# Optimization experiments

Measured on AMD Instinct MI355X. Metric: run time of the kernel, lower is better.

The kernel has to match this reference:

```python
import jax, jax.numpy as jnp
import numpy as np

B, S, D, H = 4, 2048, 1024, 16
DK = D // H

def setup_inputs() -> dict:
    key = jax.random.key(0)
    ks = jax.random.split(key, 5)
    scale = 0.02
    return {
        "x": jax.random.normal(ks[0], (B, S, D), dtype=jnp.float32),
        "Wqkv": jax.random.normal(ks[1], (3 * D, D), dtype=jnp.float32) * scale,
        "bqkv": jax.random.normal(ks[2], (3 * D,), dtype=jnp.float32) * scale,
        "Wout": jax.random.normal(ks[3], (D, D), dtype=jnp.float32) * scale,
        "bout": jax.random.normal(ks[4], (D,), dtype=jnp.float32) * scale,
    }

def reference(x, Wqkv, bqkv, Wout, bout):
    # fused QKV projection: [B,S,3D]
    qkv = jnp.einsum('bsd,ed->bse', x, Wqkv) + bqkv
    q, k, v = jnp.split(qkv, 3, axis=-1)
    # [B,S,D] -> [B,H,S,DK]
    def heads(t):
        return t.reshape(B, S, H, DK).transpose(0, 2, 1, 3)
    q, k, v = heads(q), heads(k), heads(v)
    # scaled dot-product attention (no mask, no dropout)
    scores = jnp.einsum('bhqd,bhkd->bhqk', q, k) / jnp.sqrt(jnp.float32(DK))
    attn = jax.nn.softmax(scores, axis=-1)
    out = jnp.einsum('bhqk,bhkd->bhqd', attn, v)
    # merge heads -> [B,S,D]
    out = out.transpose(0, 2, 1, 3).reshape(B, S, D)
    return jnp.einsum('bsd,ed->bse', out, Wout) + bout
```

## Files before the change

kernel.cpp:

```cpp
#include <hip/hip_runtime.h>
#include <hip/hip_bf16.h>
#include <cstdint>
#include <cstddef>

typedef __bf16 bf16_t;
typedef bf16_t bf16x8 __attribute__((ext_vector_type(8)));
typedef bf16_t bf16x4 __attribute__((ext_vector_type(4)));
typedef bf16_t bf16x2 __attribute__((ext_vector_type(2)));
typedef float f32x4 __attribute__((ext_vector_type(4)));
typedef float f32x16 __attribute__((ext_vector_type(16)));
typedef unsigned int u32x4 __attribute__((ext_vector_type(4)));

#define B_  4
#define S_  2048
#define D_  1024
#define H_  16
#define DK_ 64

#define QSCALE 0.18033688011112042f

__device__ __forceinline__ void gload_lds16(const bf16_t* g, bf16_t* l) {
  __builtin_amdgcn_global_load_lds(
      (__attribute__((address_space(1))) void*)(void*)g,
      (__attribute__((address_space(3))) void*)(void*)l,
      16, 0, 0);
}

__device__ __forceinline__ f32x4 mfma_bf16(bf16x8 a, bf16x8 b, f32x4 c) {
  return __builtin_amdgcn_mfma_f32_16x16x32_bf16(a, b, c, 0, 0, 0);
}
__device__ __forceinline__ f32x16 mfma32(bf16x8 a, bf16x8 b, f32x16 c) {
  return __builtin_amdgcn_mfma_f32_32x32x16_bf16(a, b, c, 0, 0, 0);
}

__device__ __forceinline__ unsigned pk2(float a, float b) {
  bf16x2 v; v[0] = (bf16_t)a; v[1] = (bf16_t)b;
  return __builtin_bit_cast(unsigned, v);
}

__device__ __forceinline__ void pl32(unsigned &a, unsigned &b) {
  auto r = __builtin_amdgcn_permlane32_swap((int)a, (int)b, false, false);
  a = (unsigned)r[0];
  b = (unsigned)r[1];
}

__global__ void cvt_f32_bf16(const float* __restrict__ in, bf16_t* __restrict__ out, int n4) {
  int i = blockIdx.x * blockDim.x + threadIdx.x;
  if (i < n4) {
    float4 v = reinterpret_cast<const float4*>(in)[i];
    bf16x4 o;
    o[0] = (bf16_t)v.x; o[1] = (bf16_t)v.y; o[2] = (bf16_t)v.z; o[3] = (bf16_t)v.w;
    reinterpret_cast<bf16x4*>(out)[i] = o;
  }
}


__global__ __launch_bounds__(256) void gemm_qkv(
    const bf16_t* __restrict__ A, const bf16_t* __restrict__ Bm,
    const float* __restrict__ bias,
    bf16_t* __restrict__ Qf, bf16_t* __restrict__ Kf, bf16_t* __restrict__ Vf) {
  __shared__ bf16_t As[128 * 32];
  __shared__ bf16_t Bs[128 * 32];
  const int t = threadIdx.x;
  const int l = t & 63;
  const int w = t >> 6;
  const int wm = w >> 1, wn = w & 1;
  const int fr = l & 15, fh = l >> 4;
  const int bid = (int)blockIdx.x;
  const int swz = (bid & 7) * 192 + (bid >> 3);
  const int m0 = (swz / 24) * 128, n0 = (swz % 24) * 128;
  const int K = 1024;
  const int ar = t >> 2, ak = (t & 3) * 8;

  f32x4 acc[4][4] = {};

  for (int k0 = 0; k0 < K; k0 += 32) {
    gload_lds16(A + (size_t)(m0 + ar) * K + k0 + ak,        &As[t * 8]);
    gload_lds16(A + (size_t)(m0 + 64 + ar) * K + k0 + ak,   &As[2048 + t * 8]);
    gload_lds16(Bm + (size_t)(n0 + ar) * K + k0 + ak,       &Bs[t * 8]);
    gload_lds16(Bm + (size_t)(n0 + 64 + ar) * K + k0 + ak,  &Bs[2048 + t * 8]);
    __syncthreads();
    bf16x8 af[4], bfv[4];
#pragma unroll
    for (int i = 0; i < 4; ++i)
      af[i] = *reinterpret_cast<const bf16x8*>(&As[(wm * 64 + i * 16 + fr) * 32 + fh * 8]);
#pragma unroll
    for (int i = 0; i < 4; ++i)
      bfv[i] = *reinterpret_cast<const bf16x8*>(&Bs[(wn * 64 + i * 16 + fr) * 32 + fh * 8]);
#pragma unroll
    for (int mi = 0; mi < 4; ++mi)
#pragma unroll
      for (int ni = 0; ni < 4; ++ni)
        acc[mi][ni] = mfma_bf16(af[mi], bfv[ni], acc[mi][ni]);
    __syncthreads();
  }

#pragma unroll
  for (int mi = 0; mi < 4; ++mi) {
#pragma unroll
    for (int ni = 0; ni < 4; ++ni) {
      const int e = n0 + wn * 64 + ni * 16 + fr;
      const int sec = e >> 10;
      const int h = (e & 1023) >> 6, dk = e & 63;
      const float bv = bias[e];
#pragma unroll
      for (int j = 0; j < 4; ++j) {
        const int m = m0 + wm * 64 + mi * 16 + fh * 4 + j;
        const int b = m >> 11, s = m & 2047;
        const float val = acc[mi][ni][j] + bv;
        const size_t hb = (size_t)(b * H_ + h) * (S_ * DK_);
        if (sec == 2) {
          const int tv = s >> 5, tt = (s >> 4) & 1, jj = dk >> 5;
          const int lane = (dk & 31) + ((s >> 3) & 1) * 32, el = s & 7;
          Vf[hb + (size_t)((((tv * 2 + tt) * 2 + jj) * 64 + lane) * 8 + el)] = (bf16_t)val;
        } else {
          const int tq = s >> 5, d = dk >> 4;
          const int lane = (s & 31) + ((dk >> 3) & 1) * 32, el = dk & 7;
          const size_t idx = hb + (size_t)(((tq * 4 + d) * 64 + lane) * 8 + el);
          if (sec == 0) Qf[idx] = (bf16_t)(val * QSCALE);
          else          Kf[idx] = (bf16_t)val;
        }
      }
    }
  }
}

__global__ __launch_bounds__(256) void gemm_out(
    const bf16_t* __restrict__ A, const bf16_t* __restrict__ Bm,
    const float* __restrict__ bias, float* __restrict__ out) {
  __shared__ bf16_t As[128 * 32];
  __shared__ bf16_t Bs[128 * 32];
  const int t = threadIdx.x;
  const int l = t & 63;
  const int w = t >> 6;
  const int wm = w >> 1, wn = w & 1;
  const int fr = l & 15, fh = l >> 4;
  const int bid = (int)blockIdx.x;
  const int swz = (bid & 7) * 64 + (bid >> 3);
  const int m0 = (swz >> 3) * 128, n0 = (swz & 7) * 128;
  const int K = 1024;
  const int ar = t >> 2, ak = (t & 3) * 8;

  f32x4 acc[4][4] = {};

  for (int k0 = 0; k0 < K; k0 += 32) {
    gload_lds16(A + (size_t)(m0 + ar) * K + k0 + ak,        &As[t * 8]);
    gload_lds16(A + (size_t)(m0 + 64 + ar) * K + k0 + ak,   &As[2048 + t * 8]);
    gload_lds16(Bm + (size_t)(n0 + ar) * K + k0 + ak,       &Bs[t * 8]);
    gload_lds16(Bm + (size_t)(n0 + 64 + ar) * K + k0 + ak,  &Bs[2048 + t * 8]);
    __syncthreads();
    bf16x8 af[4], bfv[4];
#pragma unroll
    for (int i = 0; i < 4; ++i)
      af[i] = *reinterpret_cast<const bf16x8*>(&As[(wm * 64 + i * 16 + fr) * 32 + fh * 8]);
#pragma unroll
    for (int i = 0; i < 4; ++i)
      bfv[i] = *reinterpret_cast<const bf16x8*>(&Bs[(wn * 64 + i * 16 + fr) * 32 + fh * 8]);
#pragma unroll
    for (int mi = 0; mi < 4; ++mi)
#pragma unroll
      for (int ni = 0; ni < 4; ++ni)
        acc[mi][ni] = mfma_bf16(af[mi], bfv[ni], acc[mi][ni]);
    __syncthreads();
  }

#pragma unroll
  for (int mi = 0; mi < 4; ++mi) {
#pragma unroll
    for (int ni = 0; ni < 4; ++ni) {
      const int e = n0 + wn * 64 + ni * 16 + fr;
      const float bv = bias[e];
#pragma unroll
      for (int j = 0; j < 4; ++j) {
        const int m = m0 + wm * 64 + mi * 16 + fh * 4 + j;
        out[(size_t)m * D_ + e] = acc[mi][ni][j] + bv;
      }
    }
  }
}

__global__ __launch_bounds__(256, 4) void attn_fwd(
    const bf16_t* __restrict__ Qf, const bf16_t* __restrict__ Kf,
    const bf16_t* __restrict__ Vf, bf16_t* __restrict__ Aout) {
  const int t = threadIdx.x, l = t & 63, w = t >> 6;
  const int lq = l & 31, hi = l >> 5;
  const int bid = (int)blockIdx.x;
  const int swz = (bid & 7) * 128 + (bid >> 3);
  const int bh = swz >> 4;
  const int q0 = (swz & 15) * 128 + w * 32;
  const int b = bh >> 4, h = bh & 15;

  const bf16_t* Qh = Qf + (size_t)bh * (S_ * DK_);
  const bf16_t* Kh = Kf + (size_t)bh * (S_ * DK_) + (size_t)l * 8;
  const bf16_t* Vh = Vf + (size_t)bh * (S_ * DK_) + (size_t)l * 8;

  const int tq = q0 >> 5;
  bf16x8 qf[4];
#pragma unroll
  for (int d = 0; d < 4; ++d)
    qf[d] = *reinterpret_cast<const bf16x8*>(&Qh[(size_t)(((tq * 4 + d) * 64 + l) * 8)]);

  f32x16 oa0 = {}, oa1 = {};
  float m = -1e30f, rs = 0.f;

  bf16x8 kA0, kA1, kA2, kA3, kB0, kB1, kB2, kB3;
  kA0 = *reinterpret_cast<const bf16x8*>(&Kh[0 * 512]);
  kA1 = *reinterpret_cast<const bf16x8*>(&Kh[1 * 512]);
  kA2 = *reinterpret_cast<const bf16x8*>(&Kh[2 * 512]);
  kA3 = *reinterpret_cast<const bf16x8*>(&Kh[3 * 512]);

#define ATTN_PHASE(KC0, KC1, KC2, KC3, KN0, KN1, KN2, KN3, CUR, NXT)                      \
  {                                                                                        \
                                                               \
    KN0 = *reinterpret_cast<const bf16x8*>(&Kh[(size_t)(((NXT) * 4 + 0) * 512)]);          \
    KN1 = *reinterpret_cast<const bf16x8*>(&Kh[(size_t)(((NXT) * 4 + 1) * 512)]);          \
    KN2 = *reinterpret_cast<const bf16x8*>(&Kh[(size_t)(((NXT) * 4 + 2) * 512)]);          \
    KN3 = *reinterpret_cast<const bf16x8*>(&Kh[(size_t)(((NXT) * 4 + 3) * 512)]);          \
                                  \
    bf16x8 v00 = *reinterpret_cast<const bf16x8*>(&Vh[(size_t)((((CUR) * 2 + 0) * 2 + 0) * 512)]); \
    bf16x8 v01 = *reinterpret_cast<const bf16x8*>(&Vh[(size_t)((((CUR) * 2 + 0) * 2 + 1) * 512)]); \
    bf16x8 v10 = *reinterpret_cast<const bf16x8*>(&Vh[(size_t)((((CUR) * 2 + 1) * 2 + 0) * 512)]); \
    bf16x8 v11 = *reinterpret_cast<const bf16x8*>(&Vh[(size_t)((((CUR) * 2 + 1) * 2 + 1) * 512)]); \
    __builtin_amdgcn_s_setprio(1);                                                         \
    f32x16 cs = {};                                                                        \
    cs = mfma32(KC0, qf[0], cs);                                                           \
    cs = mfma32(KC1, qf[1], cs);                                                           \
    cs = mfma32(KC2, qf[2], cs);                                                           \
    cs = mfma32(KC3, qf[3], cs);                                                           \
    __builtin_amdgcn_s_setprio(0);                                                         \
                                                    \
    float t0 = fmaxf(fmaxf(cs[0], cs[1]), cs[2]);                                          \
    float t1 = fmaxf(fmaxf(cs[3], cs[4]), cs[5]);                                          \
    float t2 = fmaxf(fmaxf(cs[6], cs[7]), cs[8]);                                          \
    float t3 = fmaxf(fmaxf(cs[9], cs[10]), cs[11]);                                        \
    float t4 = fmaxf(fmaxf(cs[12], cs[13]), cs[14]);                                       \
    float tm = fmaxf(fmaxf(fmaxf(t0, t1), cs[15]), fmaxf(fmaxf(t2, t3), t4));              \
    if (__any(tm > m + 8.f)) {                                                             \
      _Pragma("unroll")                                                                    \
      for (int sh = 1; sh < 64; sh <<= 1) tm = fmaxf(tm, __shfl_xor(tm, sh));              \
      const float alpha = __builtin_amdgcn_exp2f(m - tm);                                  \
      m = tm; rs *= alpha;                                                                 \
      _Pragma("unroll")                                                                    \
      for (int r = 0; r < 16; ++r) { oa0[r] *= alpha; oa1[r] *= alpha; }                   \
    }                                                                                      \
    float pv[16];                                                                          \
    _Pragma("unroll")                                                                      \
    for (int r = 0; r < 16; ++r) pv[r] = __builtin_amdgcn_exp2f(cs[r] - m);                \
    {                                                                                      \
      float s0 = pv[0] + pv[1],   s1 = pv[2] + pv[3];                                      \
      float s2 = pv[4] + pv[5],   s3 = pv[6] + pv[7];                                      \
      float s4 = pv[8] + pv[9],   s5 = pv[10] + pv[11];                                    \
      float s6 = pv[12] + pv[13], s7 = pv[14] + pv[15];                                    \
      rs += ((s0 + s1) + (s2 + s3)) + ((s4 + s5) + (s6 + s7));                             \
    }                                                                                      \
    _Pragma("unroll")                                                                      \
    for (int tt = 0; tt < 2; ++tt) {                                                       \
      unsigned A0 = pk2(pv[8 * tt],     pv[8 * tt + 1]);                                   \
      unsigned B0 = pk2(pv[8 * tt + 2], pv[8 * tt + 3]);                                   \
      unsigned A1 = pk2(pv[8 * tt + 4], pv[8 * tt + 5]);                                   \
      unsigned B1 = pk2(pv[8 * tt + 6], pv[8 * tt + 7]);                                   \
      pl32(A0, A1);                                                                        \
      pl32(B0, B1);                                                                        \
      u32x4 fw;                                                                            \
      fw[0] = A0; fw[1] = B0; fw[2] = A1; fw[3] = B1;                                      \
      const bf16x8 pa = __builtin_bit_cast(bf16x8, fw);                                    \
      __builtin_amdgcn_s_setprio(1);                                                       \
      oa0 = mfma32(pa, (tt ? v10 : v00), oa0);                                             \
      oa1 = mfma32(pa, (tt ? v11 : v01), oa1);                                             \
      __builtin_amdgcn_s_setprio(0);                                                       \
    }                                                                                      \
  }

  for (int it = 0; it < 64; it += 2) {
    ATTN_PHASE(kA0, kA1, kA2, kA3, kB0, kB1, kB2, kB3, it, it + 1)
    ATTN_PHASE(kB0, kB1, kB2, kB3, kA0, kA1, kA2, kA3, it + 1, (it + 2) & 63)
  }
#undef ATTN_PHASE

  rs += __shfl_xor(rs, 32);
  const float inv = 1.0f / rs;
#pragma unroll
  for (int r = 0; r < 16; ++r) {
    const int ql = (r & 3) + 8 * (r >> 2) + 4 * hi;
    const float ir = __shfl(inv, ql);
    const size_t row = (size_t)(b * S_ + q0 + ql) * D_ + h * 64 + lq;
    Aout[row]      = (bf16_t)(oa0[r] * ir);
    Aout[row + 32] = (bf16_t)(oa1[r] * ir);
  }
}

extern "C" void kernel_launch(void* const* d_in, const int* in_sizes, int n_in,
                              void* d_out, int out_size, void* d_ws, size_t ws_size,
                              hipStream_t stream) {
  const float* x    = (const float*)d_in[0];
  const float* Wqkv = (const float*)d_in[1];
  const float* bqkv = (const float*)d_in[2];
  const float* Wout = (const float*)d_in[3];
  const float* bout = (const float*)d_in[4];
  float* out = (float*)d_out;

  char* ws = (char*)d_ws;
  bf16_t* xb    = (bf16_t*)(ws);
  bf16_t* wqkvb = (bf16_t*)(ws + 16777216);
  bf16_t* woutb = (bf16_t*)(ws + 23068672);
  bf16_t* Qfr   = (bf16_t*)(ws + 25165824);
  bf16_t* Kfr   = (bf16_t*)(ws + 41943040);
  bf16_t* Vfr   = (bf16_t*)(ws + 58720256);
  bf16_t* aout  = (bf16_t*)(ws + 75497472);

  cvt_f32_bf16<<<8192, 256, 0, stream>>>(x, xb, 2097152);
  cvt_f32_bf16<<<3072, 256, 0, stream>>>(Wqkv, wqkvb, 786432);
  cvt_f32_bf16<<<1024, 256, 0, stream>>>(Wout, woutb, 262144);

  gemm_qkv<<<1536, 256, 0, stream>>>(xb, wqkvb, bqkv, Qfr, Kfr, Vfr);
  attn_fwd<<<1024, 256, 0, stream>>>(Qfr, Kfr, Vfr, aout);
  gemm_out<<<512, 256, 0, stream>>>(aout, woutb, bout, out);
}
```

Baseline: 204.3 us.

## Pipeline GEMM K-loop with 4-stage async LDS buffers and XOR swizzle

Both projection GEMMs now keep four LDS stages of A/B tiles filled by direct global-to-LDS loads issued three tiles ahead. Explicit vmcnt waits and raw barriers replace the load-sync-compute-sync loop, and an XOR swizzle on the column index is meant to reduce LDS bank conflicts on the fragment reads. The MFMA block is raised to high priority. This is meant to hide global memory latency behind MFMA work, at the cost of four times the LDS per block (64 KB), which limits occupancy to about two blocks per CU.

Result: slower. 214.0 us (+4.7%).

```diff
diff --git a/kernel.cpp b/kernel.cpp
--- a/kernel.cpp
+++ b/kernel.cpp
@@ -55,12 +55,45 @@
 }
 
 
-__global__ __launch_bounds__(256) void gemm_qkv(
+#define GEMM_STAGE(KT, Aptr, Bptr)                                                          \
+  {                                                                                         \
+    const int bq_ = (KT) & 3;                                                               \
+    gload_lds16((Aptr) + (size_t)(m0 + ar) * 1024 + (KT) * 32 + xcol,      &As[bq_][t * 8]);        \
+    gload_lds16((Aptr) + (size_t)(m0 + 64 + ar) * 1024 + (KT) * 32 + xcol, &As[bq_][2048 + t * 8]); \
+    gload_lds16((Bptr) + (size_t)(n0 + ar) * 1024 + (KT) * 32 + xcol,      &Bs[bq_][t * 8]);        \
+    gload_lds16((Bptr) + (size_t)(n0 + 64 + ar) * 1024 + (KT) * 32 + xcol, &Bs[bq_][2048 + t * 8]); \
+  }
+
+#define GEMM_COMPUTE(KT)                                                                    \
+  {                                                                                         \
+    __builtin_amdgcn_s_barrier();                                                           \
+    asm volatile("" ::: "memory");                                                          \
+    const bf16_t* Ab_ = &As[(KT) & 3][0];                                                   \
+    const bf16_t* Bb_ = &Bs[(KT) & 3][0];                                                   \
+    bf16x8 af[4], bfv[4];                                                                   \
+    _Pragma("unroll")                                                                       \
+    for (int i = 0; i < 4; ++i)                                                             \
+      af[i] = *reinterpret_cast<const bf16x8*>(&Ab_[(wm * 64 + i * 16 + fr) * 32 + xrd]);   \
+    _Pragma("unroll")                                                                       \
+    for (int i = 0; i < 4; ++i)                                                             \
+      bfv[i] = *reinterpret_cast<const bf16x8*>(&Bb_[(wn * 64 + i * 16 + fr) * 32 + xrd]);  \
+    __builtin_amdgcn_s_setprio(1);                                                          \
+    _Pragma("unroll")                                                                       \
+    for (int mi = 0; mi < 4; ++mi)                                                          \
+      _Pragma("unroll")                                                                     \
+      for (int ni = 0; ni < 4; ++ni)                                                        \
+        acc[mi][ni] = mfma_bf16(af[mi], bfv[ni], acc[mi][ni]);                              \
+    __builtin_amdgcn_s_setprio(0);                                                          \
+    asm volatile("" ::: "memory");                                                          \
+    __builtin_amdgcn_s_barrier();                                                           \
+  }
+
+__global__ __launch_bounds__(256, 2) void gemm_qkv(
     const bf16_t* __restrict__ A, const bf16_t* __restrict__ Bm,
     const float* __restrict__ bias,
     bf16_t* __restrict__ Qf, bf16_t* __restrict__ Kf, bf16_t* __restrict__ Vf) {
-  __shared__ bf16_t As[128 * 32];
-  __shared__ bf16_t Bs[128 * 32];
+  __shared__ bf16_t As[4][128 * 32];
+  __shared__ bf16_t Bs[4][128 * 32];
   const int t = threadIdx.x;
   const int l = t & 63;
   const int w = t >> 6;
@@ -69,31 +102,26 @@
   const int bid = (int)blockIdx.x;
   const int swz = (bid & 7) * 192 + (bid >> 3);
   const int m0 = (swz / 24) * 128, n0 = (swz % 24) * 128;
-  const int K = 1024;
-  const int ar = t >> 2, ak = (t & 3) * 8;
+  const int ar = t >> 2;
+  const int xcol = (((t & 3) ^ ((ar >> 1) & 3)) * 8);
+  const int xrd  = ((fh ^ ((fr >> 1) & 3)) * 8);
 
   f32x4 acc[4][4] = {};
 
-  for (int k0 = 0; k0 < K; k0 += 32) {
-    gload_lds16(A + (size_t)(m0 + ar) * K + k0 + ak,        &As[t * 8]);
-    gload_lds16(A + (size_t)(m0 + 64 + ar) * K + k0 + ak,   &As[2048 + t * 8]);
-    gload_lds16(Bm + (size_t)(n0 + ar) * K + k0 + ak,       &Bs[t * 8]);
-    gload_lds16(Bm + (size_t)(n0 + 64 + ar) * K + k0 + ak,  &Bs[2048 + t * 8]);
-    __syncthreads();
-    bf16x8 af[4], bfv[4];
-#pragma unroll
-    for (int i = 0; i < 4; ++i)
-      af[i] = *reinterpret_cast<const bf16x8*>(&As[(wm * 64 + i * 16 + fr) * 32 + fh * 8]);
-#pragma unroll
-    for (int i = 0; i < 4; ++i)
-      bfv[i] = *reinterpret_cast<const bf16x8*>(&Bs[(wn * 64 + i * 16 + fr) * 32 + fh * 8]);
-#pragma unroll
-    for (int mi = 0; mi < 4; ++mi)
-#pragma unroll
-      for (int ni = 0; ni < 4; ++ni)
-        acc[mi][ni] = mfma_bf16(af[mi], bfv[ni], acc[mi][ni]);
-    __syncthreads();
-  }
+  GEMM_STAGE(0, A, Bm)
+  GEMM_STAGE(1, A, Bm)
+  GEMM_STAGE(2, A, Bm)
+  for (int kt = 0; kt < 29; ++kt) {
+    GEMM_STAGE(kt + 3, A, Bm)
+    asm volatile("s_waitcnt vmcnt(12)" ::: "memory");
+    GEMM_COMPUTE(kt)
+  }
+  asm volatile("s_waitcnt vmcnt(8)" ::: "memory");
+  GEMM_COMPUTE(29)
+  asm volatile("s_waitcnt vmcnt(4)" ::: "memory");
+  GEMM_COMPUTE(30)
+  asm volatile("s_waitcnt vmcnt(0)" ::: "memory");
+  GEMM_COMPUTE(31)
 
 #pragma unroll
   for (int mi = 0; mi < 4; ++mi) {
@@ -125,11 +153,11 @@
   }
 }
 
-__global__ __launch_bounds__(256) void gemm_out(
+__global__ __launch_bounds__(256, 2) void gemm_out(
     const bf16_t* __restrict__ A, const bf16_t* __restrict__ Bm,
     const float* __restrict__ bias, float* __restrict__ out) {
-  __shared__ bf16_t As[128 * 32];
-  __shared__ bf16_t Bs[128 * 32];
+  __shared__ bf16_t As[4][128 * 32];
+  __shared__ bf16_t Bs[4][128 * 32];
   const int t = threadIdx.x;
   const int l = t & 63;
   const int w = t >> 6;
@@ -138,31 +166,26 @@
   const int bid = (int)blockIdx.x;
   const int swz = (bid & 7) * 64 + (bid >> 3);
   const int m0 = (swz >> 3) * 128, n0 = (swz & 7) * 128;
-  const int K = 1024;
-  const int ar = t >> 2, ak = (t & 3) * 8;
+  const int ar = t >> 2;
+  const int xcol = (((t & 3) ^ ((ar >> 1) & 3)) * 8);
+  const int xrd  = ((fh ^ ((fr >> 1) & 3)) * 8);
 
   f32x4 acc[4][4] = {};
 
-  for (int k0 = 0; k0 < K; k0 += 32) {
-    gload_lds16(A + (size_t)(m0 + ar) * K + k0 + ak,        &As[t * 8]);
-    gload_lds16(A + (size_t)(m0 + 64 + ar) * K + k0 + ak,   &As[2048 + t * 8]);
-    gload_lds16(Bm + (size_t)(n0 + ar) * K + k0 + ak,       &Bs[t * 8]);
-    gload_lds16(Bm + (size_t)(n0 + 64 + ar) * K + k0 + ak,  &Bs[2048 + t * 8]);
-    __syncthreads();
-    bf16x8 af[4], bfv[4];
-#pragma unroll
-    for (int i = 0; i < 4; ++i)
-      af[i] = *reinterpret_cast<const bf16x8*>(&As[(wm * 64 + i * 16 + fr) * 32 + fh * 8]);
-#pragma unroll
-    for (int i = 0; i < 4; ++i)
-      bfv[i] = *reinterpret_cast<const bf16x8*>(&Bs[(wn * 64 + i * 16 + fr) * 32 + fh * 8]);
-#pragma unroll
-    for (int mi = 0; mi < 4; ++mi)
-#pragma unroll
-      for (int ni = 0; ni < 4; ++ni)
-        acc[mi][ni] = mfma_bf16(af[mi], bfv[ni], acc[mi][ni]);
-    __syncthreads();
-  }
+  GEMM_STAGE(0, A, Bm)
+  GEMM_STAGE(1, A, Bm)
+  GEMM_STAGE(2, A, Bm)
+  for (int kt = 0; kt < 29; ++kt) {
+    GEMM_STAGE(kt + 3, A, Bm)
+    asm volatile("s_waitcnt vmcnt(12)" ::: "memory");
+    GEMM_COMPUTE(kt)
+  }
+  asm volatile("s_waitcnt vmcnt(8)" ::: "memory");
+  GEMM_COMPUTE(29)
+  asm volatile("s_waitcnt vmcnt(4)" ::: "memory");
+  GEMM_COMPUTE(30)
+  asm volatile("s_waitcnt vmcnt(0)" ::: "memory");
+  GEMM_COMPUTE(31)
 
 #pragma unroll
   for (int mi = 0; mi < 4; ++mi) {
@@ -211,12 +234,10 @@
 
 #define ATTN_PHASE(KC0, KC1, KC2, KC3, KN0, KN1, KN2, KN3, CUR, NXT)                      \
   {                                                                                        \
-                                                               \
     KN0 = *reinterpret_cast<const bf16x8*>(&Kh[(size_t)(((NXT) * 4 + 0) * 512)]);          \
     KN1 = *reinterpret_cast<const bf16x8*>(&Kh[(size_t)(((NXT) * 4 + 1) * 512)]);          \
     KN2 = *reinterpret_cast<const bf16x8*>(&Kh[(size_t)(((NXT) * 4 + 2) * 512)]);          \
     KN3 = *reinterpret_cast<const bf16x8*>(&Kh[(size_t)(((NXT) * 4 + 3) * 512)]);          \
-                                  \
     bf16x8 v00 = *reinterpret_cast<const bf16x8*>(&Vh[(size_t)((((CUR) * 2 + 0) * 2 + 0) * 512)]); \
     bf16x8 v01 = *reinterpret_cast<const bf16x8*>(&Vh[(size_t)((((CUR) * 2 + 0) * 2 + 1) * 512)]); \
     bf16x8 v10 = *reinterpret_cast<const bf16x8*>(&Vh[(size_t)((((CUR) * 2 + 1) * 2 + 0) * 512)]); \
@@ -228,7 +249,6 @@
     cs = mfma32(KC2, qf[2], cs);                                                           \
     cs = mfma32(KC3, qf[3], cs);                                                           \
     __builtin_amdgcn_s_setprio(0);                                                         \
-                                                    \
     float t0 = fmaxf(fmaxf(cs[0], cs[1]), cs[2]);                                          \
     float t1 = fmaxf(fmaxf(cs[3], cs[4]), cs[5]);                                          \
     float t2 = fmaxf(fmaxf(cs[6], cs[7]), cs[8]);                                          \
```
